# Optimization experiments

Measured on AMD Instinct MI355X. Metric: run time of the kernel, lower is better.

Reference implementation:

```python
import jax, jax.numpy as jnp
import numpy as np

B, S, H, NH = 2, 2048, 1024, 16
HD = H // NH  # head dim = 64


def setup_inputs() -> dict:
    key = jax.random.key(0)
    k_in, k_q, k_kv, k_o = jax.random.split(key, 4)
    scale = 0.02
    return {
        "inputs": jax.random.normal(k_in, (B, S, H), dtype=jnp.float32),
        "Wq": jax.random.normal(k_q, (H, H), dtype=jnp.float32) * scale,
        "bq": jnp.zeros((H,), dtype=jnp.float32),
        "Wkv": jax.random.normal(k_kv, (H, 2 * H), dtype=jnp.float32) * scale,
        "bkv": jnp.zeros((2 * H,), dtype=jnp.float32),
        "Wo": jax.random.normal(k_o, (H, H), dtype=jnp.float32) * scale,
        "bo": jnp.zeros((H,), dtype=jnp.float32),
    }


def reference(inputs, Wq, bq, Wkv, bkv, Wo, bo):
    b, s, h = inputs.shape
    q = inputs @ Wq + bq                      # [B,S,H]
    kv = inputs @ Wkv + bkv                   # [B,S,2H]
    k, v = kv[..., :h], kv[..., h:]           # each [B,S,H]
    q = q.reshape(b, s, NH, HD)
    k = k.reshape(b, s, NH, HD)
    v = v.reshape(b, s, NH, HD)
    inv_sqrt_d = jnp.asarray(1.0 / np.sqrt(HD), dtype=inputs.dtype)
    scores = jnp.einsum("bqhd,bkhd->bhqk", q, k) * inv_sqrt_d  # [B,NH,S,S]
    probs = jax.nn.softmax(scores, axis=-1)
    attended = jnp.einsum("bhqk,bkhd->bqhd", probs, v)         # [B,S,NH,HD]
    attended = attended.reshape(b, s, h)
    return attended @ Wo + bo
```

## Files before the change

### kernel.cpp

```cpp
#include <hip/hip_runtime.h>
#include <cstdint>

typedef __bf16 bf16;
typedef __attribute__((ext_vector_type(8))) __bf16 bf16x8;
typedef __attribute__((ext_vector_type(4))) __bf16 bf16v4;
typedef __attribute__((ext_vector_type(4))) float f32x4;
typedef __attribute__((ext_vector_type(16))) float f32x16;

#define MFMA16(a, b, c) __builtin_amdgcn_mfma_f32_16x16x32_bf16((a), (b), (c), 0, 0, 0)
#define MFMA32(a, b, c) __builtin_amdgcn_mfma_f32_32x32x16_bf16((a), (b), (c), 0, 0, 0)

#define BATCH 2
#define SLEN 2048
#define HDIM 1024
#define NHEAD 16
#define HEADD 64
#define MROWS (BATCH * SLEN)

#define CEXP 0.1803368801f

typedef __attribute__((address_space(3))) void lds_void;
typedef const __attribute__((address_space(1))) void glb_void;
__device__ __forceinline__ void load_lds16(const bf16* g, bf16* l) {
    __builtin_amdgcn_global_load_lds((glb_void*)g, (lds_void*)l, 16, 0, 0);
}

__global__ __launch_bounds__(256) void prep_kernel(const float* __restrict__ X,
                                                   const float* __restrict__ Wq,
                                                   const float* __restrict__ Wkv,
                                                   const float* __restrict__ Wo,
                                                   const float* __restrict__ bq,
                                                   const float* __restrict__ bkv,
                                                   bf16* __restrict__ Xbf,
                                                   bf16* __restrict__ WqkvT,
                                                   bf16* __restrict__ WoT,
                                                   float* __restrict__ bqkv) {
    const int blk = blockIdx.x;
    const int tid = threadIdx.x;
    if (blk < 4096) {
        int i = (blk * 256 + tid) * 4;
        float4 v = *(const float4*)&X[i];
        bf16v4 o;
        o[0] = (bf16)v.x; o[1] = (bf16)v.y; o[2] = (bf16)v.z; o[3] = (bf16)v.w;
        *(bf16v4*)&Xbf[i] = o;
        return;
    }
    if (blk < 8192) {
        const float* in; bf16* out; int C, id;
        if (blk < 5120)      { in = Wq;  out = WqkvT;                C = 1024; id = blk - 4096; }
        else if (blk < 7168) { in = Wkv; out = WqkvT + 1024 * 1024;  C = 2048; id = blk - 5120; }
        else                 { in = Wo;  out = WoT;                  C = 1024; id = blk - 7168; }
        const int R = 1024;
        const int nbx = C / 32;
        const int j0 = (id % nbx) * 32, i0 = (id / nbx) * 32;
        const int tx = tid & 31, ty = tid >> 5;
        __shared__ float t[32][33];
        for (int r = ty; r < 32; r += 8)
            t[r][tx] = in[(size_t)(i0 + r) * C + j0 + tx];
        __syncthreads();
        for (int r = ty; r < 32; r += 8)
            out[(size_t)(j0 + r) * R + i0 + tx] = (bf16)t[tx][r];
        return;
    }
    int i = (blk - 8192) * 256 + tid;
    if (i < 3072) bqkv[i] = (i < 1024) ? bq[i] : bkv[i - 1024];
}

template <int BM, int BN, int EPI>
__global__ __launch_bounds__(256) void gemm2_kernel(const bf16* __restrict__ A,
                                                    const bf16* __restrict__ BT,
                                                    const float* __restrict__ bias,
                                                    bf16* __restrict__ oQ,
                                                    bf16* __restrict__ oK,
                                                    bf16* __restrict__ oVT,
                                                    float* __restrict__ oF, int K) {
    constexpr int WM = BM / 2, WN = BN / 2;
    constexpr int MT = WM / 16, NT = WN / 16;

    const int tid = threadIdx.x;
    const int lane = tid & 63, wid = tid >> 6;
    const int l15 = lane & 15, quad = lane >> 4;
    const int wm = (wid >> 1) * WM, wn = (wid & 1) * WN;
    const int m0 = blockIdx.y * BM, n0 = blockIdx.x * BN;

    __shared__ bf16 As[BM * 32];
    __shared__ bf16 Bs[BN * 32];

    f32x4 acc[MT][NT] = {};

    const bf16* Ag = A + (size_t)m0 * K;
    const bf16* Bg = BT + (size_t)n0 * K;
    const int arow = lane >> 2, acol = (lane & 3) * 8;

    for (int k0 = 0; k0 < K; k0 += 32) {
#pragma unroll
        for (int t = 0; t < BM / 64; ++t) {
            int tt = t * 4 + wid;
            load_lds16(Ag + (size_t)(tt * 16 + arow) * K + k0 + acol, &As[tt * 512]);
        }
#pragma unroll
        for (int t = 0; t < BN / 64; ++t) {
            int tt = t * 4 + wid;
            load_lds16(Bg + (size_t)(tt * 16 + arow) * K + k0 + acol, &Bs[tt * 512]);
        }
        __syncthreads();

        bf16x8 af[MT], bfr[NT];
#pragma unroll
        for (int i = 0; i < MT; ++i)
            af[i] = *(const bf16x8*)&As[(wm + i * 16 + l15) * 32 + quad * 8];
#pragma unroll
        for (int j = 0; j < NT; ++j)
            bfr[j] = *(const bf16x8*)&Bs[(wn + j * 16 + l15) * 32 + quad * 8];
#pragma unroll
        for (int i = 0; i < MT; ++i)
#pragma unroll
            for (int j = 0; j < NT; ++j)
                acc[i][j] = MFMA16(af[i], bfr[j], acc[i][j]);
        __syncthreads();
    }

#pragma unroll
    for (int i = 0; i < MT; ++i) {
#pragma unroll
        for (int j = 0; j < NT; ++j) {
            const int mb = m0 + wm + i * 16 + quad * 4;
            const int n = n0 + wn + j * 16 + l15;
            const float bv = bias[n];
            if (EPI == 2) {
                float* o = oF + (size_t)mb * 1024 + n;
#pragma unroll
                for (int r = 0; r < 4; ++r) o[(size_t)r * 1024] = acc[i][j][r] + bv;
            } else if (n0 < 1024) {
#pragma unroll
                for (int r = 0; r < 4; ++r)
                    oQ[(size_t)(mb + r) * 1024 + n] = (bf16)((acc[i][j][r] + bv) * CEXP);
            } else if (n0 < 2048) {
#pragma unroll
                for (int r = 0; r < 4; ++r)
                    oK[(size_t)(mb + r) * 1024 + (n - 1024)] = (bf16)(acc[i][j][r] + bv);
            } else {
                const int hd = n - 2048;
                const int bb = mb >> 11, ss = mb & 2047;
                bf16v4 pk;
#pragma unroll
                for (int r = 0; r < 4; ++r) pk[r] = (bf16)(acc[i][j][r] + bv);
                *(bf16v4*)&oVT[((size_t)(bb << 10) + hd) * 2048 + ss] = pk;
            }
        }
    }
}

__global__ __launch_bounds__(256) void attn6_kernel(const bf16* __restrict__ Q,
                                                    const bf16* __restrict__ K,
                                                    const bf16* __restrict__ VT,
                                                    bf16* __restrict__ O) {
    const int bid = blockIdx.x;
    const int xcd = bid & 7, j = bid >> 3;
    const int bh = xcd * 4 + (j >> 4);
    const int q0 = (j & 15) * 128;
    const int b = bh >> 4, head = bh & 15;
    const int tid = threadIdx.x;
    const int lane = tid & 63, wid = tid >> 6;
    const int l31 = lane & 31, hh = lane >> 5;

    __shared__ bf16 Ks[128 * 64];
    __shared__ bf16 VTs[64 * 128];
    __shared__ bf16 Ps[4][32 * 72];

    const int qw = q0 + wid * 32;
    bf16x8 qf[4];
#pragma unroll
    for (int kd = 0; kd < 4; ++kd)
        qf[kd] = *(const bf16x8*)&Q[(size_t)(b * SLEN + qw + l31) * HDIM +
                                    head * 64 + kd * 16 + hh * 8];

    f32x16 o_acc[2] = {};
    float l_lane = 0.f;

    const bf16* Kg = K + (size_t)b * SLEN * HDIM + head * 64;
    const bf16* Vg = VT + (size_t)bh * 64 * SLEN;

    const int r8 = lane >> 3, p8 = lane & 7;
    const int r16 = lane >> 4, p16 = lane & 15;

    for (int kt = 0; kt < 16; ++kt) {
        const int k0 = kt * 128;
#pragma unroll
        for (int pass = 0; pass < 4; ++pass) {
            const int rbk = pass * 32 + wid * 8;
            load_lds16(Kg + (size_t)(k0 + rbk + r8) * HDIM + ((p8 ^ ((rbk + r8) & 7)) * 8),
                       &Ks[rbk * 64]);
            const int rbv = pass * 16 + wid * 4;
            load_lds16(Vg + (size_t)(rbv + r16) * SLEN + k0 + ((p16 ^ ((rbv + r16) & 15)) * 8),
                       &VTs[rbv * 128]);
        }
        __syncthreads();

#pragma unroll
        for (int h = 0; h < 2; ++h) {
            f32x16 sacc[2] = {};
#pragma unroll
            for (int kd = 0; kd < 4; ++kd)
#pragma unroll
                for (int m = 0; m < 2; ++m) {
                    const int key = (h * 2 + m) * 32 + l31;
                    const int c = (kd * 2 + hh) ^ (key & 7);
                    bf16x8 kf = *(const bf16x8*)&Ks[key * 64 + c * 8];
                    sacc[m] = MFMA32(kf, qf[kd], sacc[m]);
                }

#pragma unroll
            for (int m = 0; m < 2; ++m)
#pragma unroll
                for (int g = 0; g < 4; ++g) {
                    bf16v4 pk;
#pragma unroll
                    for (int r = 0; r < 4; ++r) {
                        float p = __builtin_amdgcn_exp2f(sacc[m][g * 4 + r]);
                        l_lane += p;
                        pk[r] = (bf16)p;
                    }
                    *(bf16v4*)&Ps[wid][l31 * 72 + m * 32 + g * 8 + 4 * hh] = pk;
                }

#pragma unroll
            for (int kstep = 0; kstep < 4; ++kstep) {
                bf16x8 pf = *(const bf16x8*)&Ps[wid][l31 * 72 + kstep * 16 + hh * 8];
#pragma unroll
                for (int dt = 0; dt < 2; ++dt) {
                    const int d = dt * 32 + l31;
                    const int cc = ((h * 4 + kstep) * 2 + hh) ^ (d & 15);
                    bf16x8 vf = *(const bf16x8*)&VTs[d * 128 + cc * 8];
                    o_acc[dt] = MFMA32(vf, pf, o_acc[dt]);
                }
            }
        }
        __syncthreads();
    }

    const float l_full = l_lane + __shfl_xor(l_lane, 32, 64);
    const float inv = 1.f / l_full;
    bf16* orow = O + (size_t)(b * SLEN + qw + l31) * HDIM + head * 64;
#pragma unroll
    for (int mt = 0; mt < 2; ++mt)
#pragma unroll
        for (int g = 0; g < 4; ++g) {
            bf16v4 pk;
#pragma unroll
            for (int r = 0; r < 4; ++r) pk[r] = (bf16)(o_acc[mt][g * 4 + r] * inv);
            *(bf16v4*)&orow[mt * 32 + g * 8 + 4 * hh] = pk;
        }
}

extern "C" void kernel_launch(void* const* d_in, const int* in_sizes, int n_in,
                              void* d_out, int out_size, void* d_ws, size_t ws_size,
                              hipStream_t stream) {
    const float* X   = (const float*)d_in[0];
    const float* Wq  = (const float*)d_in[1];
    const float* bq  = (const float*)d_in[2];
    const float* Wkv = (const float*)d_in[3];
    const float* bkv = (const float*)d_in[4];
    const float* Wo  = (const float*)d_in[5];
    const float* bo  = (const float*)d_in[6];
    float* out = (float*)d_out;

    char* ws = (char*)d_ws;
    bf16* Xbf   = (bf16*)(ws);
    bf16* WqkvT = (bf16*)(ws + (8ull << 20));
    bf16* WoT   = (bf16*)(ws + (14ull << 20));
    float* bqkv = (float*)(ws + (16ull << 20));
    bf16* Qbf   = (bf16*)(ws + (17ull << 20));
    bf16* Kbf   = (bf16*)(ws + (25ull << 20));
    bf16* VTbf  = (bf16*)(ws + (33ull << 20));
    bf16* Abf   = (bf16*)(ws + (41ull << 20));

    prep_kernel<<<8204, 256, 0, stream>>>(X, Wq, Wkv, Wo, bq, bkv, Xbf, WqkvT, WoT, bqkv);

    gemm2_kernel<128, 128, 1><<<dim3(3072 / 128, MROWS / 128), 256, 0, stream>>>(
        Xbf, WqkvT, bqkv, Qbf, Kbf, VTbf, nullptr, 1024);

    attn6_kernel<<<512, 256, 0, stream>>>(Qbf, Kbf, VTbf, Abf);

    gemm2_kernel<128, 64, 2><<<dim3(1024 / 64, MROWS / 128), 256, 0, stream>>>(
        Abf, WoT, bo, nullptr, nullptr, nullptr, out, 1024);
}
```

Baseline: 198.2 us.

## Split attention key tiles across wave pairs and pass P through registers

The attention kernel now handles 64 queries per block instead of 128, so it launches twice as many blocks. Within a block, two waves share each 32-query group and each wave processes half of every 128-key tile. The partial O accumulators and row sums are then combined through LDS at the end. The P matrix no longer round-trips through a per-wave LDS buffer: bf16 probabilities are repacked into the MFMA B-operand layout with a cross-half lane shuffle, and launch bounds request 4 blocks per CU. This aims to raise occupancy and parallelism and cut LDS traffic, at the cost of reloading K/V tiles in twice as many blocks and adding a final reduction step.

```diff
diff --git a/kernel.cpp b/kernel.cpp
--- a/kernel.cpp
+++ b/kernel.cpp
@@ -151,24 +151,28 @@
     }
 }
 
-__global__ __launch_bounds__(256) void attn6_kernel(const bf16* __restrict__ Q,
-                                                    const bf16* __restrict__ K,
-                                                    const bf16* __restrict__ VT,
-                                                    bf16* __restrict__ O) {
+__global__ __launch_bounds__(256, 4) void attn7_kernel(const bf16* __restrict__ Q,
+                                                       const bf16* __restrict__ K,
+                                                       const bf16* __restrict__ VT,
+                                                       bf16* __restrict__ O) {
     const int bid = blockIdx.x;
     const int xcd = bid & 7, j = bid >> 3;
-    const int bh = xcd * 4 + (j >> 4);
-    const int q0 = (j & 15) * 128;
+    const int bh = xcd * 4 + (j >> 5);
+    const int q0 = (j & 31) * 64;
     const int b = bh >> 4, head = bh & 15;
     const int tid = threadIdx.x;
     const int lane = tid & 63, wid = tid >> 6;
     const int l31 = lane & 31, hh = lane >> 5;
-
-    __shared__ bf16 Ks[128 * 64];
-    __shared__ bf16 VTs[64 * 128];
-    __shared__ bf16 Ps[4][32 * 72];
-
-    const int qw = q0 + wid * 32;
+    const int qgroup = wid & 1, khalf = wid >> 1;
+
+    __shared__ union SMem {
+        struct { bf16 Ks[128 * 64]; bf16 VTs[64 * 128]; } t;
+        float Xs[8192];
+    } sm;
+    bf16* Ks = sm.t.Ks;
+    bf16* VTs = sm.t.VTs;
+
+    const int qw = q0 + qgroup * 32;
     bf16x8 qf[4];
 #pragma unroll
     for (int kd = 0; kd < 4; ++kd)
@@ -176,13 +180,15 @@
                                     head * 64 + kd * 16 + hh * 8];
 
     f32x16 o_acc[2] = {};
-    float l_lane = 0.f;
+    float lp0 = 0.f, lp1 = 0.f, lp2 = 0.f, lp3 = 0.f;
 
     const bf16* Kg = K + (size_t)b * SLEN * HDIM + head * 64;
     const bf16* Vg = VT + (size_t)bh * 64 * SLEN;
 
     const int r8 = lane >> 3, p8 = lane & 7;
     const int r16 = lane >> 4, p16 = lane & 15;
+    const int kb = khalf * 64;
+    const int sw7 = l31 & 7, sw15 = l31 & 15;
 
     for (int kt = 0; kt < 16; ++kt) {
         const int k0 = kt * 128;
@@ -197,60 +203,96 @@
         }
         __syncthreads();
 
-#pragma unroll
-        for (int h = 0; h < 2; ++h) {
-            f32x16 sacc[2] = {};
-#pragma unroll
-            for (int kd = 0; kd < 4; ++kd)
-#pragma unroll
-                for (int m = 0; m < 2; ++m) {
-                    const int key = (h * 2 + m) * 32 + l31;
-                    const int c = (kd * 2 + hh) ^ (key & 7);
-                    bf16x8 kf = *(const bf16x8*)&Ks[key * 64 + c * 8];
-                    sacc[m] = MFMA32(kf, qf[kd], sacc[m]);
-                }
-
-#pragma unroll
-            for (int m = 0; m < 2; ++m)
-#pragma unroll
-                for (int g = 0; g < 4; ++g) {
-                    bf16v4 pk;
-#pragma unroll
-                    for (int r = 0; r < 4; ++r) {
-                        float p = __builtin_amdgcn_exp2f(sacc[m][g * 4 + r]);
-                        l_lane += p;
-                        pk[r] = (bf16)p;
-                    }
-                    *(bf16v4*)&Ps[wid][l31 * 72 + m * 32 + g * 8 + 4 * hh] = pk;
-                }
-
-#pragma unroll
-            for (int kstep = 0; kstep < 4; ++kstep) {
-                bf16x8 pf = *(const bf16x8*)&Ps[wid][l31 * 72 + kstep * 16 + hh * 8];
-#pragma unroll
-                for (int dt = 0; dt < 2; ++dt) {
-                    const int d = dt * 32 + l31;
-                    const int cc = ((h * 4 + kstep) * 2 + hh) ^ (d & 15);
-                    bf16x8 vf = *(const bf16x8*)&VTs[d * 128 + cc * 8];
-                    o_acc[dt] = MFMA32(vf, pf, o_acc[dt]);
-                }
-            }
-        }
-        __syncthreads();
-    }
-
-    const float l_full = l_lane + __shfl_xor(l_lane, 32, 64);
-    const float inv = 1.f / l_full;
-    bf16* orow = O + (size_t)(b * SLEN + qw + l31) * HDIM + head * 64;
-#pragma unroll
-    for (int mt = 0; mt < 2; ++mt)
-#pragma unroll
-        for (int g = 0; g < 4; ++g) {
-            bf16v4 pk;
-#pragma unroll
-            for (int r = 0; r < 4; ++r) pk[r] = (bf16)(o_acc[mt][g * 4 + r] * inv);
-            *(bf16v4*)&orow[mt * 32 + g * 8 + 4 * hh] = pk;
-        }
+        f32x16 sacc[2] = {};
+#pragma unroll
+        for (int kd = 0; kd < 4; ++kd)
+#pragma unroll
+            for (int m = 0; m < 2; ++m) {
+                const int key = kb + m * 32 + l31;
+                const int c = (kd * 2 + hh) ^ sw7;
+                bf16x8 kf = *(const bf16x8*)&Ks[key * 64 + c * 8];
+                sacc[m] = MFMA32(kf, qf[kd], sacc[m]);
+            }
+
+#pragma unroll
+        for (int m = 0; m < 2; ++m)
+#pragma unroll
+            for (int g = 0; g < 4; ++g) {
+                float p0 = __builtin_amdgcn_exp2f(sacc[m][g * 4 + 0]);
+                float p1 = __builtin_amdgcn_exp2f(sacc[m][g * 4 + 1]);
+                float p2 = __builtin_amdgcn_exp2f(sacc[m][g * 4 + 2]);
+                float p3 = __builtin_amdgcn_exp2f(sacc[m][g * 4 + 3]);
+                lp0 += p0; lp1 += p1; lp2 += p2; lp3 += p3;
+                sacc[m][g * 4 + 0] = p0; sacc[m][g * 4 + 1] = p1;
+                sacc[m][g * 4 + 2] = p2; sacc[m][g * 4 + 3] = p3;
+            }
+
+#pragma unroll
+        for (int s = 0; s < 4; ++s) {
+            const int m = s >> 1, base = 8 * (s & 1);
+            bf16v4 lo4, hi4;
+#pragma unroll
+            for (int r = 0; r < 4; ++r) {
+                lo4[r] = (bf16)sacc[m][base + r];
+                hi4[r] = (bf16)sacc[m][base + 4 + r];
+            }
+            uint2 lo = __builtin_bit_cast(uint2, lo4);
+            uint2 hi = __builtin_bit_cast(uint2, hi4);
+            unsigned s0 = hh ? lo.x : hi.x;
+            unsigned s1 = hh ? lo.y : hi.y;
+            unsigned r0 = __shfl_xor(s0, 32, 64);
+            unsigned r1 = __shfl_xor(s1, 32, 64);
+            uint4 f;
+            f.x = hh ? r0 : lo.x;
+            f.y = hh ? r1 : lo.y;
+            f.z = hh ? hi.x : r0;
+            f.w = hh ? hi.y : r1;
+            bf16x8 pf = __builtin_bit_cast(bf16x8, f);
+#pragma unroll
+            for (int dt = 0; dt < 2; ++dt) {
+                const int d = dt * 32 + l31;
+                const int cc = (khalf * 8 + s * 2 + hh) ^ sw15;
+                bf16x8 vf = *(const bf16x8*)&VTs[d * 128 + cc * 8];
+                o_acc[dt] = MFMA32(vf, pf, o_acc[dt]);
+            }
+        }
+        __syncthreads();
+    }
+
+    float l_lane = (lp0 + lp1) + (lp2 + lp3);
+    l_lane += __shfl_xor(l_lane, 32, 64);
+
+    float* Xs = sm.Xs;
+    if (khalf == 1) {
+        float* w = Xs + qgroup * 2304 + lane * 36;
+#pragma unroll
+        for (int mt = 0; mt < 2; ++mt)
+#pragma unroll
+            for (int g = 0; g < 4; ++g) {
+                f32x4 v = {o_acc[mt][g * 4 + 0], o_acc[mt][g * 4 + 1],
+                           o_acc[mt][g * 4 + 2], o_acc[mt][g * 4 + 3]};
+                *(f32x4*)&w[mt * 16 + g * 4] = v;
+            }
+        if (hh == 0) Xs[4608 + qgroup * 32 + l31] = l_lane;
+    }
+    __syncthreads();
+    if (khalf == 0) {
+        const float* w = Xs + qgroup * 2304 + lane * 36;
+        const float l_full = l_lane + Xs[4608 + qgroup * 32 + l31];
+        const float inv = 1.f / l_full;
+        bf16* orow = O + (size_t)(b * SLEN + qw + l31) * HDIM + head * 64;
+#pragma unroll
+        for (int mt = 0; mt < 2; ++mt)
+#pragma unroll
+            for (int g = 0; g < 4; ++g) {
+                f32x4 v = *(const f32x4*)&w[mt * 16 + g * 4];
+                bf16v4 pk;
+#pragma unroll
+                for (int r = 0; r < 4; ++r)
+                    pk[r] = (bf16)((o_acc[mt][g * 4 + r] + v[r]) * inv);
+                *(bf16v4*)&orow[mt * 32 + g * 8 + 4 * hh] = pk;
+            }
+    }
 }
 
 extern "C" void kernel_launch(void* const* d_in, const int* in_sizes, int n_in,
@@ -280,7 +322,7 @@
     gemm2_kernel<128, 128, 1><<<dim3(3072 / 128, MROWS / 128), 256, 0, stream>>>(
         Xbf, WqkvT, bqkv, Qbf, Kbf, VTbf, nullptr, 1024);
 
-    attn6_kernel<<<512, 256, 0, stream>>>(Qbf, Kbf, VTbf, Abf);
+    attn7_kernel<<<1024, 256, 0, stream>>>(Qbf, Kbf, VTbf, Abf);
 
     gemm2_kernel<128, 64, 2><<<dim3(1024 / 64, MROWS / 128), 256, 0, stream>>>(
         Abf, WoT, bo, nullptr, nullptr, nullptr, out, 1024);
```

Result: slower. 205.1 us (+3.5%).
